# Optimization experiments

Measured on AMD Instinct MI355X. Metric: run time of the kernel, lower is better.

Reference implementation:

```python
import jax, jax.numpy as jnp
import numpy as np

K_TOP = 4  # C_output
EPS = 1e-5


def setup_inputs() -> dict:
    N, C, H = 3072, 16, 128
    key = jax.random.key(0)
    ks = jax.random.split(key, 6)
    s = 1.0 / np.sqrt(H)
    return {
        "input_embedding": jax.random.normal(ks[0], (N, C, H), jnp.float32),
        "W1": jax.random.normal(ks[1], (H, H), jnp.float32) * s,
        "b1": jnp.zeros((H,), jnp.float32),
        "ln_g": jnp.ones((H,), jnp.float32),
        "ln_b": jnp.zeros((H,), jnp.float32),
        "W2": jax.random.normal(ks[2], (1, H), jnp.float32) * s,
        "b2": jnp.zeros((1,), jnp.float32),
        "sage_Wl": jax.random.normal(ks[3], (C, H, H), jnp.float32) * s,
        "sage_bl": jnp.zeros((C, H), jnp.float32),
        "sage_Wr": jax.random.normal(ks[4], (C, H, H), jnp.float32) * s,
    }


def _forward(input_embedding, W1, b1, ln_g, ln_b, W2, b2, sage_Wl, sage_bl, sage_Wr):
    n, c, h = input_embedding.shape
    # ---- feature importance learner (single shared MLP, dropout in eval) ----
    z = jax.nn.relu(jnp.einsum('nch,oh->nco', input_embedding, W1) + b1)
    mu = z.mean(-1, keepdims=True)
    var = z.var(-1, keepdims=True)  # biased, matches torch LayerNorm
    z = (z - mu) / jnp.sqrt(var + EPS) * ln_g + ln_b
    fi = jax.nn.softmax((jnp.einsum('nch,oh->nco', z, W2) + b2)[..., 0], axis=1)  # [N,C]

    feat = input_embedding * fi[:, :, None]  # importance-weighted embeddings [N,C,H]

    # ---- top-K column routing per row ----
    _, topk_idx = jax.lax.top_k(fi, K_TOP)                                    # [N,K]
    mask = jnp.zeros((n, c), bool).at[jnp.arange(n)[:, None], topk_idx].set(True)
    imp = jax.nn.softmax(jnp.where(mask, fi, -1e9), axis=1)                   # [N,C]

    col_ids = jnp.arange(c)

    # ---- per-column dynamic graph + SAGEConv (scan over C columns) ----
    def col_step(_, xs):
        ci, feat_c, cmask, Wl, bl, Wr = xs  # feat_c [N,H], cmask [N] bool
        cm = cmask.astype(feat_c.dtype)
        # subset rows whose topK contains column ci; zero out column ci
        Mc = jnp.where(col_ids[None, :] == ci, 0.0, imp) * cm[:, None]        # [N,C]
        A = (Mc @ Mc.T > 0).astype(feat_c.dtype)                              # [N,N] edges
        deg = A.sum(axis=1)
        agg = (A @ feat_c) / jnp.maximum(deg, 1.0)[:, None]                   # mean aggr
        hc = agg @ Wl.T + bl + feat_c @ Wr.T                                  # SAGEConv
        hc = jax.nn.relu(hc)
        # torch.layer_norm(x, x.shape): normalize over the whole subset tensor
        m = cm[:, None]
        n_el = jnp.maximum(cm.sum() * h, 1.0)
        mu_ = (hc * m).sum() / n_el
        var_ = (((hc - mu_) ** 2) * m).sum() / n_el
        hc = (hc - mu_) / jnp.sqrt(var_ + EPS)
        return None, hc

    _, H_all = jax.lax.scan(
        col_step, None,
        (col_ids, feat.transpose(1, 0, 2), mask.T, sage_Wl, sage_bl, sage_Wr))  # [C,N,H]

    # ---- regroup: per row, its K routed columns in ascending column order ----
    cols_sorted = jnp.sort(topk_idx, axis=1)                                  # [N,K]
    out = H_all[cols_sorted, jnp.arange(n)[:, None], :]                       # [N,K,H]
    return out


def reference(input_embedding, W1, b1, ln_g, ln_b, W2, b2, sage_Wl, sage_bl, sage_Wr):
    return _forward(input_embedding, W1, b1, ln_g, ln_b, W2, b2,
                    sage_Wl, sage_bl, sage_Wr)
```

## Files before the change

kernel.cpp:

```cpp
#include <hip/hip_runtime.h>
#include <hip/hip_bf16.h>

#define NN 3072
#define CCC 16
#define HH 128
#define KTOP 4
#define NCLS 455
#define NUP 120
#define EPSF 1e-5f

#define OFF_F       0
#define SZ_F        (16*NCLS*HH)
#define OFF_CNT     (OFF_F + SZ_F)
#define SZ_CNT      (16*NCLS)
#define OFF_SUMS    (OFF_CNT + SZ_CNT)
#define SZ_SUMS     32
#define OFF_NCNT    (OFF_SUMS + SZ_SUMS)
#define SZ_NCNT     256
#define ZERO_FLOATS (OFF_NCNT + SZ_NCNT)
#define OFF_LOGITS  ZERO_FLOATS
#define SZ_LOGITS   (NN*CCC)
#define OFF_COLS    (OFF_LOGITS + SZ_LOGITS)
#define SZ_E        (NN*KTOP)
#define OFF_RANKS   (OFF_COLS + SZ_E)
#define OFF_FISEL   (OFF_RANKS + SZ_E)
#define OFF_NLIST   (OFF_FISEL + SZ_E)
#define SZ_NLIST    (16*NN)
#define OFF_UP      (OFF_NLIST + SZ_NLIST)
#define SZ_UP       (16*NUP*HH)
#define OFF_AGG     (OFF_UP + SZ_UP)
#define OFF_HC      (OFF_AGG + SZ_F)
#define SZ_HC       (NN*KTOP*HH)
#define OFF_HALF    (OFF_HC + SZ_HC)
#define HOFF_W1H    0
#define HOFF_W1L    16384
#define HOFF_WLH    32768
#define HOFF_WRH    (32768 + 262144)
#define CVT_TOTAL   (16384 + 262144 + 262144)

typedef _Float16 h8 __attribute__((ext_vector_type(8)));
typedef float    f4 __attribute__((ext_vector_type(4)));

__device__ __forceinline__ int C2i(int x){ return x*(x-1)/2; }
__device__ __forceinline__ int C3i(int x){ return x*(x-1)*(x-2)/6; }

#define MT 64

__global__ __launch_bounds__(256) void k_cvt(const float* __restrict__ W1,
    const float* __restrict__ Wl, const float* __restrict__ Wr,
    _Float16* __restrict__ hbase, float* __restrict__ ws){
  int i = blockIdx.x*256 + threadIdx.x;
  if (i < ZERO_FLOATS) ws[i] = 0.f;
  if (i < 16384){
    float x = W1[i];
    _Float16 h = (_Float16)x;
    hbase[HOFF_W1H + i] = h;
    hbase[HOFF_W1L + i] = (_Float16)(x - (float)h);
  }
  int j = i - 16384;
  if (j >= 0 && j < 262144) hbase[HOFF_WLH + j] = (_Float16)Wl[j];
  int k2 = i - (16384 + 262144);
  if (k2 >= 0 && k2 < 262144) hbase[HOFF_WRH + k2] = (_Float16)Wr[k2];
}

__global__ __launch_bounds__(256) void k_logits(const float* __restrict__ X,
    const _Float16* __restrict__ W1h, const _Float16* __restrict__ W1l,
    const float* __restrict__ b1, const float* __restrict__ ln_g,
    const float* __restrict__ ln_b, const float* __restrict__ W2,
    const float* __restrict__ b2, float* __restrict__ logits){
  int t = threadIdx.x;
  int w = t >> 6;
  int lane = t & 63;
  int l15 = lane & 15, quad = lane >> 4;
  int base = blockIdx.x * MT;
  int mA = base + 16*w + l15;

  const float* xrow = X + (size_t)mA*HH;
  h8 ah[4], al[4];
  #pragma unroll
  for (int c=0;c<4;++c){
    float4 u = *(const float4*)(xrow + c*32 + quad*8);
    float4 v = *(const float4*)(xrow + c*32 + quad*8 + 4);
    float xv[8] = {u.x,u.y,u.z,u.w,v.x,v.y,v.z,v.w};
    #pragma unroll
    for (int j=0;j<8;++j){
      _Float16 hi = (_Float16)xv[j];
      ah[c][j] = hi;
      al[c][j] = (_Float16)(xv[j] - (float)hi);
    }
  }

  f4 acc[8];
  #pragma unroll
  for (int nt=0;nt<8;++nt) acc[nt] = (f4){0.f,0.f,0.f,0.f};

  #pragma unroll
  for (int c=0;c<4;++c){
    #pragma unroll
    for (int nt=0;nt<8;++nt){
      int o = nt*16 + l15;
      h8 bh  = *(const h8*)(W1h + (size_t)o*HH + c*32 + quad*8);
      h8 bl_ = *(const h8*)(W1l + (size_t)o*HH + c*32 + quad*8);
      acc[nt] = __builtin_amdgcn_mfma_f32_16x16x32_f16(ah[c], bh,  acc[nt], 0,0,0);
      acc[nt] = __builtin_amdgcn_mfma_f32_16x16x32_f16(al[c], bh,  acc[nt], 0,0,0);
      acc[nt] = __builtin_amdgcn_mfma_f32_16x16x32_f16(ah[c], bl_, acc[nt], 0,0,0);
      acc[nt] = __builtin_amdgcn_mfma_f32_16x16x32_f16(al[c], bl_, acc[nt], 0,0,0);
    }
  }

  float bv[8], gv[8], lv[8], wv[8];
  #pragma unroll
  for (int nt=0;nt<8;++nt){
    int o = nt*16 + l15;
    bv[nt]=b1[o]; gv[nt]=ln_g[o]; lv[nt]=ln_b[o]; wv[nt]=W2[o];
  }
  float b2v = b2[0];
  #pragma unroll
  for (int r=0;r<4;++r){
    float z[8];
    float s1=0.f, s2=0.f;
    #pragma unroll
    for (int nt=0;nt<8;++nt){
      float zz = acc[nt][r] + bv[nt];
      zz = zz>0.f ? zz : 0.f;
      z[nt] = zz; s1 += zz; s2 += zz*zz;
    }
    #pragma unroll
    for (int m=1;m<16;m<<=1){ s1 += __shfl_xor(s1,m); s2 += __shfl_xor(s2,m); }
    float mu = s1/(float)HH;
    float var = s2/(float)HH - mu*mu;
    float rs = 1.0f/sqrtf(var+EPSF);
    float s3 = 0.f;
    #pragma unroll
    for (int nt=0;nt<8;++nt){
      float zn = (z[nt]-mu)*rs*gv[nt] + lv[nt];
      s3 += zn*wv[nt];
    }
    #pragma unroll
    for (int m=1;m<16;m<<=1) s3 += __shfl_xor(s3,m);
    if (l15 == 0) logits[base + 16*w + quad*4 + r] = s3 + b2v;
  }
}

__global__ __launch_bounds__(256) void k_topk(const float* __restrict__ logits,
    int* __restrict__ cols, int* __restrict__ ranks, float* __restrict__ fiSel,
    int* __restrict__ nodeCnt, int* __restrict__ nodeList){
  __shared__ int lcnt[CCC];
  __shared__ int lbase[CCC];
  int t = threadIdx.x;
  if (t < CCC) lcnt[t] = 0;
  __syncthreads();
  int n = blockIdx.x*256 + t;
  float l[CCC];
  #pragma unroll
  for (int c=0;c<CCC;++c) l[c] = logits[n*CCC+c];
  unsigned mask = 0;
  #pragma unroll
  for (int k=0;k<KTOP;++k){
    float best = -3e38f; int bi = 0;
    #pragma unroll
    for (int c=0;c<CCC;++c){
      bool taken = (mask>>c)&1u;
      if (!taken && l[c] > best){ best = l[c]; bi = c; }
    }
    mask |= 1u<<bi;
  }
  float m = -3e38f;
  #pragma unroll
  for (int c=0;c<CCC;++c) m = l[c]>m ? l[c] : m;
  float s = 0.f;
  #pragma unroll
  for (int c=0;c<CCC;++c) s += expf(l[c]-m);
  float inv = 1.0f/s;
  int mycis[KTOP], mypos[KTOP];
  unsigned m2 = mask;
  for (int j=0;j<KTOP;++j){
    int ci = __ffs(m2)-1; m2 &= m2-1u;
    unsigned rest = mask & ~(1u<<ci);
    int v[3]; unsigned r2 = rest;
    #pragma unroll
    for (int q=0;q<3;++q){ int col = __ffs(r2)-1; r2 &= r2-1u; v[q] = col - (col>ci ? 1:0); }
    int rank = C3i(v[2]) + C2i(v[1]) + v[0];
    int e4 = n*KTOP + j;
    cols[e4] = ci; ranks[e4] = rank;
    fiSel[e4] = expf(l[ci]-m)*inv;
    mycis[j] = ci;
    mypos[j] = atomicAdd(&lcnt[ci], 1);
  }
  __syncthreads();
  if (t < CCC) lbase[t] = atomicAdd(&nodeCnt[t*16], lcnt[t]);
  __syncthreads();
  #pragma unroll
  for (int j=0;j<KTOP;++j){
    int ci = mycis[j];
    nodeList[ci*NN + lbase[ci] + mypos[j]] = n*KTOP + j;
  }
}

__global__ __launch_bounds__(256) void k_accF(const float* __restrict__ X,
    const int* __restrict__ cols, const int* __restrict__ ranks,
    const float* __restrict__ fiSel, float* __restrict__ F, float* __restrict__ cnt){
  int e = blockIdx.x*2 + (threadIdx.x>>7);
  int h = threadIdx.x & 127;
  int ci = cols[e], rank = ranks[e];
  float fi = fiSel[e];
  int n = e >> 2;
  float v = X[(n*CCC+ci)*HH + h] * fi;
  atomicAdd(&F[(ci*NCLS+rank)*HH + h], v);
  if (h==0) atomicAdd(&cnt[ci*NCLS+rank], 1.0f);
}

#define GCP 8
#define GCB (HH/GCP)
__global__ __launch_bounds__(256) void k_graph(const float* __restrict__ F,
    const float* __restrict__ cnt, float* __restrict__ agg){
  int cb = blockIdx.x, ci = blockIdx.y, t = threadIdx.x;
  __shared__ float cntl[NCLS];
  __shared__ float PcS[105], UcS[15];
  __shared__ int   abcs[NCLS];
  __shared__ int   prs[NCLS];
  __shared__ float Fl[NCLS*GCP];
  __shared__ float P[105*GCP];
  __shared__ float U[15*GCP];
  const float* Fc = F + (size_t)ci*NCLS*HH + cb*GCP;

  for (int i=t; i<NCLS*2; i+=256){
    int r = i>>1, hf = i&1;
    float4 v = *(const float4*)(Fc + (size_t)r*HH + hf*4);
    *(float4*)(&Fl[r*GCP + hf*4]) = v;
  }
  for (int r=t; r<NCLS; r+=256){
    cntl[r] = cnt[ci*NCLS+r];
    int c=2; while (c<14 && C3i(c+1)<=r) c++;
    int rem = r - C3i(c);
    int b=1; while (b<c-1 && C2i(b+1)<=rem) b++;
    int a = rem - C2i(b);
    abcs[r] = a | (b<<5) | (c<<10);
    prs[r] = (C2i(b)+a) | ((C2i(c)+a)<<10) | ((C2i(c)+b)<<20);
  }
  __syncthreads();
  if (t<105){
    int pb=1; while (pb<14 && C2i(pb+1)<=t) pb++;
    int pa = t - C2i(pb);
    float s=0.f;
    #pragma unroll
    for (int z=0;z<15;++z){
      if (z==pa||z==pb) continue;
      int lo,mid,hi;
      if (z<pa){lo=z;mid=pa;hi=pb;} else if (z<pb){lo=pa;mid=z;hi=pb;} else {lo=pa;mid=pb;hi=z;}
      s += cntl[C3i(hi)+C2i(mid)+lo];
    }
    PcS[t]=s;
  }
  __syncthreads();
  if (t<15){
    float s=0.f;
    #pragma unroll
    for (int y=0;y<15;++y){
      if (y==t) continue;
      int lo = t<y?t:y, hi = t<y?y:t;
      s += PcS[C2i(hi)+lo];
    }
    UcS[t]=0.5f*s;
  }
  __syncthreads();
  for (int idx=t; idx<105*GCP; idx+=256){
    int p = idx/GCP, col = idx&(GCP-1);
    int pb=1; while (pb<14 && C2i(pb+1)<=p) pb++;
    int pa = p - C2i(pb);
    float s=0.f;
    #pragma unroll
    for (int z=0;z<15;++z){
      if (z==pa||z==pb) continue;
      int lo,mid,hi;
      if (z<pa){lo=z;mid=pa;hi=pb;} else if (z<pb){lo=pa;mid=z;hi=pb;} else {lo=pa;mid=pb;hi=z;}
      s += Fl[(C3i(hi)+C2i(mid)+lo)*GCP + col];
    }
    P[idx]=s;
  }
  __syncthreads();
  for (int idx=t; idx<15*GCP; idx+=256){
    int x = idx/GCP, col = idx&(GCP-1);
    float s=0.f;
    #pragma unroll
    for (int y=0;y<15;++y){
      if (y==x) continue;
      int lo = x<y?x:y, hi = x<y?y:x;
      s += P[(C2i(hi)+lo)*GCP + col];
    }
    U[idx]=0.5f*s;
  }
  __syncthreads();
  for (int idx=t; idx<NCLS*GCP; idx+=256){
    int r = idx/GCP, col = idx&(GCP-1);
    int v1=abcs[r]; int a=v1&31,b=(v1>>5)&31,c=(v1>>10)&31;
    int v2=prs[r];  int pab=v2&1023,pac=(v2>>10)&1023,pbc=(v2>>20)&1023;
    float deg = UcS[a]+UcS[b]+UcS[c]-PcS[pab]-PcS[pac]-PcS[pbc]+cntl[r];
    float invd = 1.0f/fmaxf(deg,1.0f);
    float v = U[a*GCP+col]+U[b*GCP+col]+U[c*GCP+col]
            - P[pab*GCP+col]-P[pac*GCP+col]-P[pbc*GCP+col]
            + Fl[r*GCP+col];
    agg[(size_t)ci*NCLS*HH + (size_t)r*HH + cb*GCP + col] = v*invd;
  }
}

__global__ __launch_bounds__(256) void k_aggwl(float* __restrict__ agg,
    const _Float16* __restrict__ Wlh, const float* __restrict__ bl){
  int t = threadIdx.x;
  int w = t >> 6;
  int lane = t & 63;
  int l15 = lane & 15, quad = lane >> 4;
  int ci = blockIdx.y;
  int base = blockIdx.x * MT;
  int rowA = base + 16*w + l15; if (rowA > NCLS-1) rowA = NCLS-1;

  const float* arow = agg + ((size_t)ci*NCLS + rowA)*HH;
  h8 af[4];
  #pragma unroll
  for (int c=0;c<4;++c){
    float4 u = *(const float4*)(arow + c*32 + quad*8);
    float4 v = *(const float4*)(arow + c*32 + quad*8 + 4);
    float xv[8] = {u.x,u.y,u.z,u.w,v.x,v.y,v.z,v.w};
    #pragma unroll
    for (int j=0;j<8;++j) af[c][j] = (_Float16)xv[j];
  }

  f4 acc[8];
  #pragma unroll
  for (int nt=0;nt<8;++nt) acc[nt] = (f4){0.f,0.f,0.f,0.f};

  const _Float16* Wc = Wlh + (size_t)ci*HH*HH;
  #pragma unroll
  for (int c=0;c<4;++c){
    #pragma unroll
    for (int nt=0;nt<8;++nt){
      int o = nt*16 + l15;
      h8 bh = *(const h8*)(Wc + (size_t)o*HH + c*32 + quad*8);
      acc[nt] = __builtin_amdgcn_mfma_f32_16x16x32_f16(af[c], bh, acc[nt], 0,0,0);
    }
  }
  #pragma unroll
  for (int r=0;r<4;++r){
    int row2 = base + 16*w + quad*4 + r;
    if (row2 < NCLS){
      float* drow = agg + ((size_t)ci*NCLS + row2)*HH;
      #pragma unroll
      for (int nt=0;nt<8;++nt){
        int o = nt*16 + l15;
        drow[o] = acc[nt][r] + bl[ci*HH + o];
      }
    }
  }
}

__global__ __launch_bounds__(256) void k_hc2(const float* __restrict__ X,
    const _Float16* __restrict__ Wrh,
    const int* __restrict__ ranks, const float* __restrict__ fiSel,
    const int* __restrict__ nodeCnt, const int* __restrict__ nodeList,
    const float* __restrict__ aggwl, float* __restrict__ hcBuf, float* __restrict__ sums){
  int ci = blockIdx.y;
  int cntc = nodeCnt[ci*16];
  int base = blockIdx.x * MT;
  if (base >= cntc) return;
  __shared__ float rb[8];
  int t = threadIdx.x;
  int w = t >> 6;
  int lane = t & 63;
  int l15 = lane & 15, quad = lane >> 4;

  int pA = base + 16*w + l15;
  float fi = 0.f; int nA = 0;
  if (pA < cntc){
    int e = nodeList[ci*NN + pA];
    fi = fiSel[e]; nA = e >> 2;
  }
  const float* xrow = X + ((size_t)nA*CCC + ci)*HH;
  h8 af[4];
  #pragma unroll
  for (int c=0;c<4;++c){
    float4 u = *(const float4*)(xrow + c*32 + quad*8);
    float4 v = *(const float4*)(xrow + c*32 + quad*8 + 4);
    float xv[8] = {u.x,u.y,u.z,u.w,v.x,v.y,v.z,v.w};
    #pragma unroll
    for (int j=0;j<8;++j) af[c][j] = (_Float16)(xv[j]*fi);
  }

  f4 acc[8];
  #pragma unroll
  for (int nt=0;nt<8;++nt) acc[nt] = (f4){0.f,0.f,0.f,0.f};

  const _Float16* Wc = Wrh + (size_t)ci*HH*HH;
  #pragma unroll
  for (int c=0;c<4;++c){
    #pragma unroll
    for (int nt=0;nt<8;++nt){
      int o = nt*16 + l15;
      h8 bh = *(const h8*)(Wc + (size_t)o*HH + c*32 + quad*8);
      acc[nt] = __builtin_amdgcn_mfma_f32_16x16x32_f16(af[c], bh, acc[nt], 0,0,0);
    }
  }

  float s1 = 0.f, s2 = 0.f;
  #pragma unroll
  for (int r=0;r<4;++r){
    int pD = base + 16*w + quad*4 + r;
    int e2 = -1, rk2 = 0;
    if (pD < cntc){ e2 = nodeList[ci*NN + pD]; rk2 = ranks[e2]; }
    if (e2 >= 0){
      const float* G = aggwl + ((size_t)ci*NCLS + rk2)*HH;
      float* drow = hcBuf + (size_t)e2*HH;
      #pragma unroll
      for (int nt=0;nt<8;++nt){
        int o = nt*16 + l15;
        float vv = acc[nt][r] + G[o];
        vv = vv>0.f ? vv : 0.f;
        drow[o] = vv;
        s1 += vv; s2 += vv*vv;
      }
    }
  }
  #pragma unroll
  for (int m=1;m<64;m<<=1){ s1 += __shfl_xor(s1,m); s2 += __shfl_xor(s2,m); }
  if (lane == 0){ rb[w] = s1; rb[4+w] = s2; }
  __syncthreads();
  if (t==0){
    atomicAdd(&sums[ci],    rb[0]+rb[1]+rb[2]+rb[3]);
    atomicAdd(&sums[16+ci], rb[4]+rb[5]+rb[6]+rb[7]);
  }
}

__global__ __launch_bounds__(256) void k_out(const float* __restrict__ hcBuf,
    const int* __restrict__ cols, const int* __restrict__ nodeCnt,
    const float* __restrict__ sums, float* __restrict__ out){
  int idx = blockIdx.x*256 + threadIdx.x;
  int e = idx >> 7;
  int ci = cols[e];
  float cntf = (float)nodeCnt[ci*16];
  float nel = fmaxf(cntf * (float)HH, 1.0f);
  float mu = sums[ci]/nel;
  float var = sums[16+ci]/nel - mu*mu;
  out[idx] = (hcBuf[idx]-mu)/sqrtf(var+EPSF);
}

extern "C" void kernel_launch(void* const* d_in, const int* in_sizes, int n_in,
                              void* d_out, int out_size, void* d_ws, size_t ws_size,
                              hipStream_t stream){
  const float* X    = (const float*)d_in[0];
  const float* W1   = (const float*)d_in[1];
  const float* b1   = (const float*)d_in[2];
  const float* ln_g = (const float*)d_in[3];
  const float* ln_b = (const float*)d_in[4];
  const float* W2   = (const float*)d_in[5];
  const float* b2   = (const float*)d_in[6];
  const float* Wl   = (const float*)d_in[7];
  const float* bl   = (const float*)d_in[8];
  const float* Wr   = (const float*)d_in[9];
  float* ws = (float*)d_ws;
  float* F      = ws + OFF_F;
  float* cnt    = ws + OFF_CNT;
  float* sums   = ws + OFF_SUMS;
  int*   nodeCnt= (int*)(ws + OFF_NCNT);
  float* logits = ws + OFF_LOGITS;
  int*   cols   = (int*)(ws + OFF_COLS);
  int*   ranks  = (int*)(ws + OFF_RANKS);
  float* fiSel  = ws + OFF_FISEL;
  int*   nodeList=(int*)(ws + OFF_NLIST);
  float* agg    = ws + OFF_AGG;
  float* hcBuf  = ws + OFF_HC;
  _Float16* hbase = (_Float16*)(ws + OFF_HALF);
  float* out    = (float*)d_out;

  int cvtGrid = (ZERO_FLOATS > CVT_TOTAL ? ZERO_FLOATS : CVT_TOTAL + 255) / 256 + 1;
  k_cvt    <<<dim3(cvtGrid), dim3(256), 0, stream>>>(W1, Wl, Wr, hbase, ws);
  k_logits <<<dim3(NN*CCC/MT), dim3(256), 0, stream>>>(X, hbase+HOFF_W1H, hbase+HOFF_W1L,
                                                       b1, ln_g, ln_b, W2, b2, logits);
  k_topk   <<<dim3(NN/256), dim3(256), 0, stream>>>(logits, cols, ranks, fiSel, nodeCnt, nodeList);
  k_accF   <<<dim3(NN*KTOP/2), dim3(256), 0, stream>>>(X, cols, ranks, fiSel, F, cnt);
  k_graph  <<<dim3(GCB,16), dim3(256), 0, stream>>>(F, cnt, agg);
  k_aggwl  <<<dim3((NCLS+MT-1)/MT,16), dim3(256), 0, stream>>>(agg, hbase+HOFF_WLH, bl);
  k_hc2    <<<dim3((NN/MT),16), dim3(256), 0, stream>>>(X, hbase+HOFF_WRH, ranks, fiSel,
                                                        nodeCnt, nodeList, agg, hcBuf, sums);
  k_out    <<<dim3(NN*KTOP*HH/256), dim3(256), 0, stream>>>(hcBuf, cols, nodeCnt, sums, out);
}
```

Baseline: 173.3 us.

## Fuse logits, top-k routing and class accumulation into one kernel

Merges the logits MLP, per-row top-k/softmax selection and the atomic accumulation into class feature sums into a single kernel. Logits stay in shared memory, and each block of 4 rows does its own routing and scatter. This removes two kernel launches and the global round trip for logits. In exchange, only 4 threads of each block run the serial top-k, nodeList slots come from per-entry global atomics instead of block-aggregated ones (so list order can vary between runs), and each thread issues 8 scalar float atomics.

```diff
diff --git a/kernel.cpp b/kernel.cpp
--- a/kernel.cpp
+++ b/kernel.cpp
@@ -63,11 +63,17 @@
   if (k2 >= 0 && k2 < 262144) hbase[HOFF_WRH + k2] = (_Float16)Wr[k2];
 }
 
-__global__ __launch_bounds__(256) void k_logits(const float* __restrict__ X,
+__global__ __launch_bounds__(256) void k_fused(const float* __restrict__ X,
     const _Float16* __restrict__ W1h, const _Float16* __restrict__ W1l,
     const float* __restrict__ b1, const float* __restrict__ ln_g,
     const float* __restrict__ ln_b, const float* __restrict__ W2,
-    const float* __restrict__ b2, float* __restrict__ logits){
+    const float* __restrict__ b2,
+    int* __restrict__ cols, int* __restrict__ ranks, float* __restrict__ fiSel,
+    int* __restrict__ nodeCnt, int* __restrict__ nodeList,
+    float* __restrict__ F, float* __restrict__ cnt){
+  __shared__ float llog[64];
+  __shared__ int   eci[16], ern[16];
+  __shared__ float efi[16];
   int t = threadIdx.x;
   int w = t >> 6;
   int lane = t & 63;
@@ -138,76 +144,67 @@
     }
     #pragma unroll
     for (int m=1;m<16;m<<=1) s3 += __shfl_xor(s3,m);
-    if (l15 == 0) logits[base + 16*w + quad*4 + r] = s3 + b2v;
-  }
-}
-
-__global__ __launch_bounds__(256) void k_topk(const float* __restrict__ logits,
-    int* __restrict__ cols, int* __restrict__ ranks, float* __restrict__ fiSel,
-    int* __restrict__ nodeCnt, int* __restrict__ nodeList){
-  __shared__ int lcnt[CCC];
-  __shared__ int lbase[CCC];
-  int t = threadIdx.x;
-  if (t < CCC) lcnt[t] = 0;
-  __syncthreads();
-  int n = blockIdx.x*256 + t;
-  float l[CCC];
-  #pragma unroll
-  for (int c=0;c<CCC;++c) l[c] = logits[n*CCC+c];
-  unsigned mask = 0;
-  #pragma unroll
-  for (int k=0;k<KTOP;++k){
-    float best = -3e38f; int bi = 0;
-    #pragma unroll
-    for (int c=0;c<CCC;++c){
-      bool taken = (mask>>c)&1u;
-      if (!taken && l[c] > best){ best = l[c]; bi = c; }
-    }
-    mask |= 1u<<bi;
-  }
-  float m = -3e38f;
-  #pragma unroll
-  for (int c=0;c<CCC;++c) m = l[c]>m ? l[c] : m;
-  float s = 0.f;
-  #pragma unroll
-  for (int c=0;c<CCC;++c) s += expf(l[c]-m);
-  float inv = 1.0f/s;
-  int mycis[KTOP], mypos[KTOP];
-  unsigned m2 = mask;
-  for (int j=0;j<KTOP;++j){
-    int ci = __ffs(m2)-1; m2 &= m2-1u;
-    unsigned rest = mask & ~(1u<<ci);
-    int v[3]; unsigned r2 = rest;
-    #pragma unroll
-    for (int q=0;q<3;++q){ int col = __ffs(r2)-1; r2 &= r2-1u; v[q] = col - (col>ci ? 1:0); }
-    int rank = C3i(v[2]) + C2i(v[1]) + v[0];
-    int e4 = n*KTOP + j;
-    cols[e4] = ci; ranks[e4] = rank;
-    fiSel[e4] = expf(l[ci]-m)*inv;
-    mycis[j] = ci;
-    mypos[j] = atomicAdd(&lcnt[ci], 1);
-  }
-  __syncthreads();
-  if (t < CCC) lbase[t] = atomicAdd(&nodeCnt[t*16], lcnt[t]);
-  __syncthreads();
-  #pragma unroll
-  for (int j=0;j<KTOP;++j){
-    int ci = mycis[j];
-    nodeList[ci*NN + lbase[ci] + mypos[j]] = n*KTOP + j;
-  }
-}
-
-__global__ __launch_bounds__(256) void k_accF(const float* __restrict__ X,
-    const int* __restrict__ cols, const int* __restrict__ ranks,
-    const float* __restrict__ fiSel, float* __restrict__ F, float* __restrict__ cnt){
-  int e = blockIdx.x*2 + (threadIdx.x>>7);
-  int h = threadIdx.x & 127;
-  int ci = cols[e], rank = ranks[e];
-  float fi = fiSel[e];
-  int n = e >> 2;
-  float v = X[(n*CCC+ci)*HH + h] * fi;
-  atomicAdd(&F[(ci*NCLS+rank)*HH + h], v);
-  if (h==0) atomicAdd(&cnt[ci*NCLS+rank], 1.0f);
+    if (l15 == 0) llog[16*w + quad*4 + r] = s3 + b2v;
+  }
+  __syncthreads();
+
+  if (t < 4){
+    int n = blockIdx.x*4 + t;
+    float l[CCC];
+    #pragma unroll
+    for (int c=0;c<CCC;++c) l[c] = llog[t*16+c];
+    unsigned mask = 0;
+    #pragma unroll
+    for (int k=0;k<KTOP;++k){
+      float best = -3e38f; int bi = 0;
+      #pragma unroll
+      for (int c=0;c<CCC;++c){
+        bool taken = (mask>>c)&1u;
+        if (!taken && l[c] > best){ best = l[c]; bi = c; }
+      }
+      mask |= 1u<<bi;
+    }
+    float m = -3e38f;
+    #pragma unroll
+    for (int c=0;c<CCC;++c) m = l[c]>m ? l[c] : m;
+    float s = 0.f;
+    #pragma unroll
+    for (int c=0;c<CCC;++c) s += expf(l[c]-m);
+    float inv = 1.0f/s;
+    unsigned m2 = mask;
+    for (int j=0;j<KTOP;++j){
+      int ci = __ffs(m2)-1; m2 &= m2-1u;
+      unsigned rest = mask & ~(1u<<ci);
+      int v[3]; unsigned r2 = rest;
+      #pragma unroll
+      for (int q=0;q<3;++q){ int col = __ffs(r2)-1; r2 &= r2-1u; v[q] = col - (col>ci ? 1:0); }
+      int rank = C3i(v[2]) + C2i(v[1]) + v[0];
+      int e4 = n*KTOP + j;
+      float fi = expf(l[ci]-m)*inv;
+      cols[e4] = ci; ranks[e4] = rank; fiSel[e4] = fi;
+      int pos = atomicAdd(&nodeCnt[ci*16], 1);
+      nodeList[ci*NN + pos] = e4;
+      eci[t*4+j] = ci; ern[t*4+j] = rank; efi[t*4+j] = fi;
+    }
+  }
+  __syncthreads();
+
+  {
+    int j  = t >> 4;
+    int cg = t & 15;
+    int ci = eci[j], rank = ern[j];
+    float fi = efi[j];
+    int n = blockIdx.x*4 + (j>>2);
+    const float* xr = X + ((size_t)n*CCC + ci)*HH + cg*8;
+    float* Fr = F + ((size_t)ci*NCLS + rank)*HH + cg*8;
+    float4 u = *(const float4*)(xr);
+    float4 v = *(const float4*)(xr+4);
+    atomicAdd(&Fr[0], u.x*fi); atomicAdd(&Fr[1], u.y*fi);
+    atomicAdd(&Fr[2], u.z*fi); atomicAdd(&Fr[3], u.w*fi);
+    atomicAdd(&Fr[4], v.x*fi); atomicAdd(&Fr[5], v.y*fi);
+    atomicAdd(&Fr[6], v.z*fi); atomicAdd(&Fr[7], v.w*fi);
+    if (cg == 0) atomicAdd(&cnt[ci*NCLS+rank], 1.0f);
+  }
 }
 
 #define GCP 8
@@ -460,7 +457,6 @@
   float* cnt    = ws + OFF_CNT;
   float* sums   = ws + OFF_SUMS;
   int*   nodeCnt= (int*)(ws + OFF_NCNT);
-  float* logits = ws + OFF_LOGITS;
   int*   cols   = (int*)(ws + OFF_COLS);
   int*   ranks  = (int*)(ws + OFF_RANKS);
   float* fiSel  = ws + OFF_FISEL;
@@ -472,10 +468,10 @@
 
   int cvtGrid = (ZERO_FLOATS > CVT_TOTAL ? ZERO_FLOATS : CVT_TOTAL + 255) / 256 + 1;
   k_cvt    <<<dim3(cvtGrid), dim3(256), 0, stream>>>(W1, Wl, Wr, hbase, ws);
-  k_logits <<<dim3(NN*CCC/MT), dim3(256), 0, stream>>>(X, hbase+HOFF_W1H, hbase+HOFF_W1L,
-                                                       b1, ln_g, ln_b, W2, b2, logits);
-  k_topk   <<<dim3(NN/256), dim3(256), 0, stream>>>(logits, cols, ranks, fiSel, nodeCnt, nodeList);
-  k_accF   <<<dim3(NN*KTOP/2), dim3(256), 0, stream>>>(X, cols, ranks, fiSel, F, cnt);
+  k_fused  <<<dim3(NN*CCC/MT), dim3(256), 0, stream>>>(X, hbase+HOFF_W1H, hbase+HOFF_W1L,
+                                                       b1, ln_g, ln_b, W2, b2,
+                                                       cols, ranks, fiSel, nodeCnt, nodeList,
+                                                       F, cnt);
   k_graph  <<<dim3(GCB,16), dim3(256), 0, stream>>>(F, cnt, agg);
   k_aggwl  <<<dim3((NCLS+MT-1)/MT,16), dim3(256), 0, stream>>>(agg, hbase+HOFF_WLH, bl);
   k_hc2    <<<dim3((NN/MT),16), dim3(256), 0, stream>>>(X, hbase+HOFF_WRH, ranks, fiSel,
```

Result: slower. 220.4 us (+27.2%).

## Fuse top-k into logits kernel and move zeroing/weight conversion there

Applied to the files above, without the earlier changes.

Top-k selection, softmax and rank computation now run at the end of the logits kernel from shared memory, so the logits round-trip through global memory goes away. Zeroing F and converting Wl/Wr to fp16 move from the large conversion kernel into the fused kernel as grid-stride side work, which shrinks k_cvt to 64 blocks. The node-list build becomes a small separate kernel that reads cols. The trade-off is that the fused kernel now carries extra memory traffic per block, and only 4 threads per block do the top-k work.

```diff
diff --git a/kernel.cpp b/kernel.cpp
--- a/kernel.cpp
+++ b/kernel.cpp
@@ -1,12 +1,10 @@
 #include <hip/hip_runtime.h>
-#include <hip/hip_bf16.h>
 
 #define NN 3072
 #define CCC 16
 #define HH 128
 #define KTOP 4
 #define NCLS 455
-#define NUP 120
 #define EPSF 1e-5f
 
 #define OFF_F       0
@@ -17,18 +15,14 @@
 #define SZ_SUMS     32
 #define OFF_NCNT    (OFF_SUMS + SZ_SUMS)
 #define SZ_NCNT     256
-#define ZERO_FLOATS (OFF_NCNT + SZ_NCNT)
-#define OFF_LOGITS  ZERO_FLOATS
-#define SZ_LOGITS   (NN*CCC)
-#define OFF_COLS    (OFF_LOGITS + SZ_LOGITS)
+#define SMALL_ZERO  (SZ_CNT + SZ_SUMS + SZ_NCNT)
+#define OFF_COLS    (OFF_NCNT + SZ_NCNT)
 #define SZ_E        (NN*KTOP)
 #define OFF_RANKS   (OFF_COLS + SZ_E)
 #define OFF_FISEL   (OFF_RANKS + SZ_E)
 #define OFF_NLIST   (OFF_FISEL + SZ_E)
 #define SZ_NLIST    (16*NN)
-#define OFF_UP      (OFF_NLIST + SZ_NLIST)
-#define SZ_UP       (16*NUP*HH)
-#define OFF_AGG     (OFF_UP + SZ_UP)
+#define OFF_AGG     (OFF_NLIST + SZ_NLIST)
 #define OFF_HC      (OFF_AGG + SZ_F)
 #define SZ_HC       (NN*KTOP*HH)
 #define OFF_HALF    (OFF_HC + SZ_HC)
@@ -36,7 +30,10 @@
 #define HOFF_W1L    16384
 #define HOFF_WLH    32768
 #define HOFF_WRH    (32768 + 262144)
-#define CVT_TOTAL   (16384 + 262144 + 262144)
+
+#define MT 64
+#define GCP 8
+#define GCB (HH/GCP)
 
 typedef _Float16 h8 __attribute__((ext_vector_type(8)));
 typedef float    f4 __attribute__((ext_vector_type(4)));
@@ -44,36 +41,43 @@
 __device__ __forceinline__ int C2i(int x){ return x*(x-1)/2; }
 __device__ __forceinline__ int C3i(int x){ return x*(x-1)*(x-2)/6; }
 
-#define MT 64
-
 __global__ __launch_bounds__(256) void k_cvt(const float* __restrict__ W1,
-    const float* __restrict__ Wl, const float* __restrict__ Wr,
     _Float16* __restrict__ hbase, float* __restrict__ ws){
   int i = blockIdx.x*256 + threadIdx.x;
-  if (i < ZERO_FLOATS) ws[i] = 0.f;
   if (i < 16384){
     float x = W1[i];
     _Float16 h = (_Float16)x;
     hbase[HOFF_W1H + i] = h;
     hbase[HOFF_W1L + i] = (_Float16)(x - (float)h);
   }
-  int j = i - 16384;
-  if (j >= 0 && j < 262144) hbase[HOFF_WLH + j] = (_Float16)Wl[j];
-  int k2 = i - (16384 + 262144);
-  if (k2 >= 0 && k2 < 262144) hbase[HOFF_WRH + k2] = (_Float16)Wr[k2];
-}
-
-__global__ __launch_bounds__(256) void k_logits(const float* __restrict__ X,
+  if (i < SMALL_ZERO) ws[OFF_CNT + i] = 0.f;
+}
+
+__global__ __launch_bounds__(256) void k_fused(const float* __restrict__ X,
     const _Float16* __restrict__ W1h, const _Float16* __restrict__ W1l,
     const float* __restrict__ b1, const float* __restrict__ ln_g,
     const float* __restrict__ ln_b, const float* __restrict__ W2,
-    const float* __restrict__ b2, float* __restrict__ logits){
+    const float* __restrict__ b2,
+    const float* __restrict__ Wl, const float* __restrict__ Wr,
+    _Float16* __restrict__ hbase, float* __restrict__ F,
+    int* __restrict__ cols, int* __restrict__ ranks, float* __restrict__ fiSel){
+  __shared__ float llog[64];
   int t = threadIdx.x;
   int w = t >> 6;
   int lane = t & 63;
   int l15 = lane & 15, quad = lane >> 4;
   int base = blockIdx.x * MT;
   int mA = base + 16*w + l15;
+
+  {
+    f4 z4 = (f4){0.f,0.f,0.f,0.f};
+    for (int i = blockIdx.x*256 + t; i < SZ_F/4; i += 768*256)
+      *(f4*)(F + (size_t)i*4) = z4;
+    for (int i = blockIdx.x*256 + t; i < 2*262144; i += 768*256){
+      if (i < 262144) hbase[HOFF_WLH + i] = (_Float16)Wl[i];
+      else            hbase[HOFF_WRH + (i-262144)] = (_Float16)Wr[i-262144];
+    }
+  }
 
   const float* xrow = X + (size_t)mA*HH;
   h8 ah[4], al[4];
@@ -138,12 +142,48 @@
     }
     #pragma unroll
     for (int m=1;m<16;m<<=1) s3 += __shfl_xor(s3,m);
-    if (l15 == 0) logits[base + 16*w + quad*4 + r] = s3 + b2v;
-  }
-}
-
-__global__ __launch_bounds__(256) void k_topk(const float* __restrict__ logits,
-    int* __restrict__ cols, int* __restrict__ ranks, float* __restrict__ fiSel,
+    if (l15 == 0) llog[16*w + quad*4 + r] = s3 + b2v;
+  }
+  __syncthreads();
+
+  if (t < 4){
+    int n = blockIdx.x*4 + t;
+    float l[CCC];
+    #pragma unroll
+    for (int c=0;c<CCC;++c) l[c] = llog[t*16+c];
+    unsigned mask = 0;
+    #pragma unroll
+    for (int k=0;k<KTOP;++k){
+      float best = -3e38f; int bi = 0;
+      #pragma unroll
+      for (int c=0;c<CCC;++c){
+        bool taken = (mask>>c)&1u;
+        if (!taken && l[c] > best){ best = l[c]; bi = c; }
+      }
+      mask |= 1u<<bi;
+    }
+    float m = -3e38f;
+    #pragma unroll
+    for (int c=0;c<CCC;++c) m = l[c]>m ? l[c] : m;
+    float s = 0.f;
+    #pragma unroll
+    for (int c=0;c<CCC;++c) s += expf(l[c]-m);
+    float inv = 1.0f/s;
+    unsigned m2 = mask;
+    for (int j=0;j<KTOP;++j){
+      int ci = __ffs(m2)-1; m2 &= m2-1u;
+      unsigned rest = mask & ~(1u<<ci);
+      int v[3]; unsigned r2 = rest;
+      #pragma unroll
+      for (int q=0;q<3;++q){ int col = __ffs(r2)-1; r2 &= r2-1u; v[q] = col - (col>ci ? 1:0); }
+      int rank = C3i(v[2]) + C2i(v[1]) + v[0];
+      int e4 = n*KTOP + j;
+      cols[e4] = ci; ranks[e4] = rank; fiSel[e4] = expf(l[ci]-m)*inv;
+    }
+  }
+}
+
+__global__ __launch_bounds__(256) void k_nlist(const int* __restrict__ cols,
     int* __restrict__ nodeCnt, int* __restrict__ nodeList){
   __shared__ int lcnt[CCC];
   __shared__ int lbase[CCC];
@@ -151,39 +191,10 @@
   if (t < CCC) lcnt[t] = 0;
   __syncthreads();
   int n = blockIdx.x*256 + t;
-  float l[CCC];
-  #pragma unroll
-  for (int c=0;c<CCC;++c) l[c] = logits[n*CCC+c];
-  unsigned mask = 0;
-  #pragma unroll
-  for (int k=0;k<KTOP;++k){
-    float best = -3e38f; int bi = 0;
-    #pragma unroll
-    for (int c=0;c<CCC;++c){
-      bool taken = (mask>>c)&1u;
-      if (!taken && l[c] > best){ best = l[c]; bi = c; }
-    }
-    mask |= 1u<<bi;
-  }
-  float m = -3e38f;
-  #pragma unroll
-  for (int c=0;c<CCC;++c) m = l[c]>m ? l[c] : m;
-  float s = 0.f;
-  #pragma unroll
-  for (int c=0;c<CCC;++c) s += expf(l[c]-m);
-  float inv = 1.0f/s;
   int mycis[KTOP], mypos[KTOP];
-  unsigned m2 = mask;
+  #pragma unroll
   for (int j=0;j<KTOP;++j){
-    int ci = __ffs(m2)-1; m2 &= m2-1u;
-    unsigned rest = mask & ~(1u<<ci);
-    int v[3]; unsigned r2 = rest;
-    #pragma unroll
-    for (int q=0;q<3;++q){ int col = __ffs(r2)-1; r2 &= r2-1u; v[q] = col - (col>ci ? 1:0); }
-    int rank = C3i(v[2]) + C2i(v[1]) + v[0];
-    int e4 = n*KTOP + j;
-    cols[e4] = ci; ranks[e4] = rank;
-    fiSel[e4] = expf(l[ci]-m)*inv;
+    int ci = cols[n*KTOP+j];
     mycis[j] = ci;
     mypos[j] = atomicAdd(&lcnt[ci], 1);
   }
@@ -210,8 +221,6 @@
   if (h==0) atomicAdd(&cnt[ci*NCLS+rank], 1.0f);
 }
 
-#define GCP 8
-#define GCB (HH/GCP)
 __global__ __launch_bounds__(256) void k_graph(const float* __restrict__ F,
     const float* __restrict__ cnt, float* __restrict__ agg){
   int cb = blockIdx.x, ci = blockIdx.y, t = threadIdx.x;
@@ -460,7 +469,6 @@
   float* cnt    = ws + OFF_CNT;
   float* sums   = ws + OFF_SUMS;
   int*   nodeCnt= (int*)(ws + OFF_NCNT);
-  float* logits = ws + OFF_LOGITS;
   int*   cols   = (int*)(ws + OFF_COLS);
   int*   ranks  = (int*)(ws + OFF_RANKS);
   float* fiSel  = ws + OFF_FISEL;
@@ -470,11 +478,11 @@
   _Float16* hbase = (_Float16*)(ws + OFF_HALF);
   float* out    = (float*)d_out;
 
-  int cvtGrid = (ZERO_FLOATS > CVT_TOTAL ? ZERO_FLOATS : CVT_TOTAL + 255) / 256 + 1;
-  k_cvt    <<<dim3(cvtGrid), dim3(256), 0, stream>>>(W1, Wl, Wr, hbase, ws);
-  k_logits <<<dim3(NN*CCC/MT), dim3(256), 0, stream>>>(X, hbase+HOFF_W1H, hbase+HOFF_W1L,
-                                                       b1, ln_g, ln_b, W2, b2, logits);
-  k_topk   <<<dim3(NN/256), dim3(256), 0, stream>>>(logits, cols, ranks, fiSel, nodeCnt, nodeList);
+  k_cvt    <<<dim3(64), dim3(256), 0, stream>>>(W1, hbase, ws);
+  k_fused  <<<dim3(NN*CCC/MT), dim3(256), 0, stream>>>(X, hbase+HOFF_W1H, hbase+HOFF_W1L,
+                                                       b1, ln_g, ln_b, W2, b2, Wl, Wr,
+                                                       hbase, F, cols, ranks, fiSel);
+  k_nlist  <<<dim3(NN/256), dim3(256), 0, stream>>>(cols, nodeCnt, nodeList);
   k_accF   <<<dim3(NN*KTOP/2), dim3(256), 0, stream>>>(X, cols, ranks, fiSel, F, cnt);
   k_graph  <<<dim3(GCB,16), dim3(256), 0, stream>>>(F, cnt, agg);
   k_aggwl  <<<dim3((NCLS+MT-1)/MT,16), dim3(256), 0, stream>>>(agg, hbase+HOFF_WLH, bl);
```

New measurement: 175.5 us. About the same (+1.3%).
